# Kernel tuning notes

Measured on AMD Instinct MI355X. Metric: run time of the kernel, lower is better.

Reference implementation:

```python
import jax, jax.numpy as jnp
import numpy as np

H = 1024   # hidden_size
NH = 16    # num heads
DH = H // NH
L = 2      # attention levels
E = 8      # experts
F = 4 * H  # expert FFN hidden
B = 2
S = 1024
EPS = 1e-5
TOPK = 2
STD = 0.02


def setup_inputs() -> dict:
    key = jax.random.key(0)
    ks = jax.random.split(key, 12)
    def n(k, shp):
        return jax.random.normal(k, shp, jnp.float32) * STD
    return {
        "hidden_states": jax.random.normal(ks[0], (B, S, H), jnp.float32),
        "attention_mask": jnp.ones((B, S), jnp.int32),
        "ln1_g": jnp.ones((H,), jnp.float32), "ln1_b": jnp.zeros((H,), jnp.float32),
        "ln2_g": jnp.ones((H,), jnp.float32), "ln2_b": jnp.zeros((H,), jnp.float32),
        "Wq": n(ks[1], (L, H, H)), "Wk": n(ks[2], (L, H, H)),
        "Wv": n(ks[3], (L, H, H)), "Wo": n(ks[4], (L, H, H)),
        "bq": jnp.zeros((L, H), jnp.float32), "bk": jnp.zeros((L, H), jnp.float32),
        "bv": jnp.zeros((L, H), jnp.float32), "bo": jnp.zeros((L, H), jnp.float32),
        "level_logits": n(ks[5], (L,)),
        "Wr": n(ks[6], (H, E)), "br": jnp.zeros((E,), jnp.float32),
        "W1": n(ks[7], (E, H, F)), "b1": jnp.zeros((E, F), jnp.float32),
        "W2": n(ks[8], (E, F, H)), "b2": jnp.zeros((E, H), jnp.float32),
    }


def _ln(x, g, b):
    m = x.mean(-1, keepdims=True)
    v = x.var(-1, keepdims=True)
    return (x - m) * jax.lax.rsqrt(v + EPS) * g + b


def _mla(x, mask_f, Wq, Wk, Wv, Wo, bq, bk, bv, bo, level_logits):
    # Multi-level attention: one MHA per level, softmax-combined over levels.
    b_, s_, _ = x.shape
    def proj(W, bias):
        y = jnp.einsum('bsh,lhd->lbsd', x, W) + bias[:, None, None, :]
        return y.reshape(L, b_, s_, NH, DH)
    q, k, v = proj(Wq, bq), proj(Wk, bk), proj(Wv, bv)
    scores = jnp.einsum('lbqnd,lbknd->lbnqk', q, k) / np.float32(np.sqrt(DH))
    bias = (1.0 - mask_f)[None, :, None, None, :] * jnp.float32(-1e9)  # key-side mask
    attn = jax.nn.softmax(scores + bias, axis=-1)
    ctx = jnp.einsum('lbnqk,lbknd->lbqnd', attn, v).reshape(L, b_, s_, H)
    out = jnp.einsum('lbsh,lhd->lbsd', ctx, Wo) + bo[:, None, None, :]
    w = jax.nn.softmax(level_logits)
    return jnp.einsum('l,lbsd->bsd', w, out)


def _moe(x, Wr, br, W1, b1, W2, b2):
    # Top-2 softmax router with renormalized gates; dense expert compute,
    # sparse combine (math-equivalent to dispatch/combine without dropping).
    logits = x @ Wr + br                                  # [B,S,E]
    probs = jax.nn.softmax(logits, axis=-1)
    topv, topi = jax.lax.top_k(probs, TOPK)               # [B,S,K]
    gates = topv / topv.sum(-1, keepdims=True)
    combine = jnp.sum(jax.nn.one_hot(topi, E, dtype=x.dtype) * gates[..., None], axis=-2)  # [B,S,E]
    h = jax.nn.gelu(jnp.einsum('bsh,ehf->besf', x, W1) + b1[None, :, None, :])
    y = jnp.einsum('besf,efh->besh', h, W2) + b2[None, :, None, :]
    return jnp.einsum('bse,besh->bsh', combine, y), logits


def reference(hidden_states, attention_mask, ln1_g, ln1_b, ln2_g, ln2_b,
              Wq, Wk, Wv, Wo, bq, bk, bv, bo, level_logits,
              Wr, br, W1, b1, W2, b2):
    mask_f = attention_mask.astype(jnp.float32)
    attn = _mla(_ln(hidden_states, ln1_g, ln1_b), mask_f,
                Wq, Wk, Wv, Wo, bq, bk, bv, bo, level_logits)
    x = hidden_states + attn                  # residual 1 (dropout in eval = identity)
    moe_out, _router_logits = _moe(_ln(x, ln2_g, ln2_b), Wr, br, W1, b1, W2, b2)
    return x + moe_out                        # residual 2
```

## Files before the change

kernel.cpp:

```cpp
#include <hip/hip_runtime.h>
#include <hip/hip_bf16.h>
#include <stdint.h>

#define Hn   1024
#define NHn  16
#define DHn  64
#define Ln   2
#define En   8
#define Fn   4096
#define Bn   2
#define Sn   1024
#define Tn   2048
#define An   4096
#define KSPLIT 4

typedef __bf16 bf16_t;
typedef __bf16 bf16x8 __attribute__((ext_vector_type(8)));
typedef float  f32x4  __attribute__((ext_vector_type(4)));

__device__ __forceinline__ f32x4 mfma16(bf16x8 a, bf16x8 b, f32x4 c){
  return __builtin_amdgcn_mfma_f32_16x16x32_bf16(a, b, c, 0, 0, 0);
}
__device__ __forceinline__ void gload16(const void* gsrc, void* ldst){
  __builtin_amdgcn_global_load_lds((const __attribute__((address_space(1))) void*)gsrc,
                                   (__attribute__((address_space(3))) void*)ldst, 16, 0, 0);
}
__device__ __forceinline__ float gelu_f(float x){
  float u = 0.7978845608028654f * (x + 0.044715f * x * x * x);
  return 0.5f * x * (1.0f + tanhf(u));
}

__global__ __launch_bounds__(256)
void tcvt_k(const float* __restrict__ src, bf16_t* __restrict__ dst, int R, int C){
  __shared__ float tile[32][33];
  size_t moff = (size_t)blockIdx.z * R * C;
  src += moff; dst += moff;
  int c0 = blockIdx.x * 32, r0 = blockIdx.y * 32;
  int tx = threadIdx.x & 31, ty = threadIdx.x >> 5;
  #pragma unroll
  for (int i = 0; i < 32; i += 8)
    tile[ty + i][tx] = src[(size_t)(r0 + ty + i) * C + (c0 + tx)];
  __syncthreads();
  #pragma unroll
  for (int i = 0; i < 32; i += 8)
    dst[(size_t)(c0 + ty + i) * R + (r0 + tx)] = (bf16_t)tile[tx][ty + i];
}

__global__ __launch_bounds__(256)
void ln_k(const float* __restrict__ x, const float* __restrict__ gam,
          const float* __restrict__ bet, bf16_t* __restrict__ out){
  int row = blockIdx.x;
  const float4* xr = (const float4*)(x + (size_t)row * Hn);
  int t = threadIdx.x, lane = t & 63, w = t >> 6;
  float4 v = xr[t];
  float s  = v.x + v.y + v.z + v.w;
  float ss = v.x*v.x + v.y*v.y + v.z*v.z + v.w*v.w;
  #pragma unroll
  for (int mk = 1; mk < 64; mk <<= 1){ s += __shfl_xor(s, mk); ss += __shfl_xor(ss, mk); }
  __shared__ float r1[4], r2[4];
  if (lane == 0){ r1[w] = s; r2[w] = ss; }
  __syncthreads();
  float S1 = r1[0]+r1[1]+r1[2]+r1[3];
  float S2 = r2[0]+r2[1]+r2[2]+r2[3];
  float mean = S1 * (1.0f/Hn);
  float var  = S2 * (1.0f/Hn) - mean*mean;
  float rstd = rsqrtf(var + 1e-5f);
  int c = t * 4;
  bf16_t* o = out + (size_t)row * Hn + c;
  o[0] = (bf16_t)((v.x-mean)*rstd*gam[c+0] + bet[c+0]);
  o[1] = (bf16_t)((v.y-mean)*rstd*gam[c+1] + bet[c+1]);
  o[2] = (bf16_t)((v.z-mean)*rstd*gam[c+2] + bet[c+2]);
  o[3] = (bf16_t)((v.w-mean)*rstd*gam[c+3] + bet[c+3]);
}

__global__ __launch_bounds__(256)
void res_ln2_k(const float* __restrict__ x, const float* __restrict__ o0,
               const float* __restrict__ o1, const float* __restrict__ lvl,
               const float* __restrict__ gam, const float* __restrict__ bet,
               float* __restrict__ x2, bf16_t* __restrict__ xn2){
  int row = blockIdx.x, t = threadIdx.x, lane = t & 63, w = t >> 6;
  float l0 = lvl[0], l1 = lvl[1];
  float mx = fmaxf(l0, l1);
  float e0 = __expf(l0 - mx), e1 = __expf(l1 - mx);
  float inv = 1.f / (e0 + e1);
  float w0 = e0 * inv, w1 = e1 * inv;
  size_t base = (size_t)row * Hn;
  float4 xv = ((const float4*)(x  + base))[t];
  float4 a0 = ((const float4*)(o0 + base))[t];
  float4 a1 = ((const float4*)(o1 + base))[t];
  float4 v;
  v.x = xv.x + w0*a0.x + w1*a1.x;
  v.y = xv.y + w0*a0.y + w1*a1.y;
  v.z = xv.z + w0*a0.z + w1*a1.z;
  v.w = xv.w + w0*a0.w + w1*a1.w;
  ((float4*)(x2 + base))[t] = v;
  float s  = v.x + v.y + v.z + v.w;
  float ss = v.x*v.x + v.y*v.y + v.z*v.z + v.w*v.w;
  #pragma unroll
  for (int mk = 1; mk < 64; mk <<= 1){ s += __shfl_xor(s, mk); ss += __shfl_xor(ss, mk); }
  __shared__ float r1[4], r2[4];
  if (lane == 0){ r1[w] = s; r2[w] = ss; }
  __syncthreads();
  float S1 = r1[0]+r1[1]+r1[2]+r1[3];
  float S2 = r2[0]+r2[1]+r2[2]+r2[3];
  float mean = S1 * (1.0f/Hn);
  float var  = S2 * (1.0f/Hn) - mean*mean;
  float rstd = rsqrtf(var + 1e-5f);
  int c = t * 4;
  bf16_t* o = xn2 + base + c;
  o[0] = (bf16_t)((v.x-mean)*rstd*gam[c+0] + bet[c+0]);
  o[1] = (bf16_t)((v.y-mean)*rstd*gam[c+1] + bet[c+1]);
  o[2] = (bf16_t)((v.z-mean)*rstd*gam[c+2] + bet[c+2]);
  o[3] = (bf16_t)((v.w-mean)*rstd*gam[c+3] + bet[c+3]);
}

struct GP {
  const bf16_t* A;
  const bf16_t* Bt;
  const float*  bias;
  float*        fout;
  bf16_t*       bfout;
  const int*    list;
  const int*    counts;
  int Kstride;
  int Kloc;
};

template<int MODE>
__global__ __launch_bounds__(256)
void gemm_k(GP p){
  const int nt = blockIdx.x, mt = blockIdx.y, z = blockIdx.z;
  const bf16_t* A = p.A;
  const bf16_t* Bt = p.Bt;
  const float* bias = p.bias;
  const int* list = nullptr;
  int cnt = 0x7fffffff;
  int kbase = 0;
  if constexpr (MODE == 0){
    Bt += (size_t)z*Hn*Hn; bias += z*Hn;
  } else if constexpr (MODE == 1){
    Bt += (size_t)z*Hn*Hn; bias += z*Hn; A += (size_t)z*Bn*Sn*Hn;
  } else if constexpr (MODE == 3){
    cnt = p.counts[z];
    if (mt * 128 >= cnt) return;
    list = p.list + z * Tn;
    Bt += (size_t)z*Fn*Hn; bias += z*Fn;
  } else {
    int e = z >> 2;
    cnt = p.counts[e];
    if (mt * 128 >= cnt) return;
    list = p.list + e * Tn;
    Bt += (size_t)e*Hn*Fn; bias += e*Hn;
    kbase = (z & 3) * (Fn / KSPLIT);
  }
  const int Ks = p.Kstride;
  const int NT = p.Kloc >> 5;

  __shared__ bf16_t As[2][128*32];
  __shared__ bf16_t Bs[2][128*32];
  const int tid = threadIdx.x, lane = tid & 63, w = tid >> 6;
  const int wr = (w >> 1) * 64, wc = (w & 1) * 64;
  const int lane15 = lane & 15, kg = lane >> 4;

  const bf16_t* aptr[2];
  const bf16_t* bptr[2];
  int chunks[2];
  #pragma unroll
  for (int i = 0; i < 2; ++i){
    int ch = w*64 + lane + i*256;
    chunks[i] = ch;
    int row = ch >> 2, kc = (ch & 3) * 8;
    int ar;
    if constexpr (MODE == 3){ int g = mt*128 + row; if (g >= cnt) g = cnt - 1; ar = list[g] >> 1; }
    else if constexpr (MODE == 4){ int g = mt*128 + row; if (g >= cnt) g = cnt - 1; ar = list[g]; }
    else ar = mt*128 + row;
    aptr[i] = A  + (size_t)ar * Ks + kbase + kc;
    bptr[i] = Bt + (size_t)(nt*128 + row) * Ks + kbase + kc;
  }

  const f32x4 fz = {0.f,0.f,0.f,0.f};
  f32x4 acc[4][4];
  #pragma unroll
  for (int m = 0; m < 4; ++m)
    #pragma unroll
    for (int n = 0; n < 4; ++n) acc[m][n] = fz;

  #pragma unroll
  for (int i = 0; i < 2; ++i){
    gload16(aptr[i], &As[0][chunks[i]*8]);
    gload16(bptr[i], &Bs[0][chunks[i]*8]);
  }
  __syncthreads();

  int cur = 0;
  for (int t = 0; t < NT; ++t){
    if (t + 1 < NT){
      int k1 = (t+1) * 32;
      #pragma unroll
      for (int i = 0; i < 2; ++i){
        gload16(aptr[i] + k1, &As[cur^1][chunks[i]*8]);
        gload16(bptr[i] + k1, &Bs[cur^1][chunks[i]*8]);
      }
    }
    bf16x8 af[4], bfr[4];
    #pragma unroll
    for (int m = 0; m < 4; ++m) af[m]  = *(const bf16x8*)(&As[cur][(wr + m*16 + lane15)*32 + kg*8]);
    #pragma unroll
    for (int n = 0; n < 4; ++n) bfr[n] = *(const bf16x8*)(&Bs[cur][(wc + n*16 + lane15)*32 + kg*8]);
    #pragma unroll
    for (int m = 0; m < 4; ++m)
      #pragma unroll
      for (int n = 0; n < 4; ++n)
        acc[m][n] = mfma16(af[m], bfr[n], acc[m][n]);
    __syncthreads();
    cur ^= 1;
  }

  if constexpr (MODE == 0){
    bf16_t* outp = p.bfout + (size_t)z * (Bn*NHn*Sn*DHn);
    #pragma unroll
    for (int m = 0; m < 4; ++m){
      int row0 = mt*128 + wr + m*16 + kg*4;
      #pragma unroll
      for (int n = 0; n < 4; ++n){
        int col = nt*128 + wc + n*16 + lane15;
        int nh = col >> 6, dh = col & 63;
        float bv = bias[col];
        f32x4 v = acc[m][n];
        #pragma unroll
        for (int r = 0; r < 4; ++r){
          int tk = row0 + r;
          int bb = tk >> 10, s = tk & 1023;
          outp[((size_t)(bb*NHn + nh)*Sn + s)*DHn + dh] = (bf16_t)(v[r] + bv);
        }
      }
    }
  } else if constexpr (MODE == 1){
    float* outp = p.fout + (size_t)z * Tn * Hn;
    #pragma unroll
    for (int m = 0; m < 4; ++m){
      int row0 = mt*128 + wr + m*16 + kg*4;
      #pragma unroll
      for (int n = 0; n < 4; ++n){
        int col = nt*128 + wc + n*16 + lane15;
        float bv = bias[col];
        f32x4 v = acc[m][n];
        #pragma unroll
        for (int r = 0; r < 4; ++r)
          outp[(size_t)(row0 + r)*Hn + col] = v[r] + bv;
      }
    }
  } else if constexpr (MODE == 3){
    #pragma unroll
    for (int m = 0; m < 4; ++m){
      int row0 = mt*128 + wr + m*16 + kg*4;
      #pragma unroll
      for (int n = 0; n < 4; ++n){
        int col = nt*128 + wc + n*16 + lane15;
        float bv = bias[col];
        f32x4 v = acc[m][n];
        #pragma unroll
        for (int r = 0; r < 4; ++r){
          int g = row0 + r;
          if (g < cnt){
            int aid = list[g];
            p.bfout[(size_t)aid*Fn + col] = (bf16_t)gelu_f(v[r] + bv);
          }
        }
      }
    }
  } else {
    float* outp = p.fout + (size_t)(z & 3) * An * Hn;
    bool addb = (z & 3) == 0;
    #pragma unroll
    for (int m = 0; m < 4; ++m){
      int row0 = mt*128 + wr + m*16 + kg*4;
      #pragma unroll
      for (int n = 0; n < 4; ++n){
        int col = nt*128 + wc + n*16 + lane15;
        float bv = addb ? bias[col] : 0.f;
        f32x4 v = acc[m][n];
        #pragma unroll
        for (int r = 0; r < 4; ++r){
          int g = row0 + r;
          if (g < cnt){
            int aid = list[g];
            outp[(size_t)aid*Hn + col] = v[r] + bv;
          }
        }
      }
    }
  }
}

__global__ __launch_bounds__(64)
void attn_k(const bf16_t* __restrict__ qh, const bf16_t* __restrict__ kh,
            const bf16_t* __restrict__ vh, const int* __restrict__ amask,
            bf16_t* __restrict__ ctxb){
  int qt = blockIdx.x;
  int z  = blockIdx.y;
  int lvl = z >> 5, bb = (z >> 4) & 1, nh = z & 15;
  int lane = threadIdx.x;
  int lane15 = lane & 15, kg = lane >> 4;
  const bf16_t* Q  = qh + (size_t)z * Sn * DHn;
  const bf16_t* Kp = kh + (size_t)z * Sn * DHn;
  const bf16_t* Vp = vh + (size_t)z * Sn * DHn;
  const int* mrow = amask + bb * Sn;
  __shared__ bf16_t p_lds[16*32];
  __shared__ bf16_t vt[64*32];
  const f32x4 fz = {0.f,0.f,0.f,0.f};
  int qr = qt*16 + lane15;
  bf16x8 qa0 = *(const bf16x8*)(Q + (size_t)qr*DHn + kg*8);
  bf16x8 qa1 = *(const bf16x8*)(Q + (size_t)qr*DHn + 32 + kg*8);
  f32x4 ctxa[4] = {fz, fz, fz, fz};
  float m_r[4] = {-1e30f,-1e30f,-1e30f,-1e30f};
  float s_r[4] = {0.f,0.f,0.f,0.f};
  int vr = lane >> 1, c0 = (lane & 1) * 32;
  for (int kc = 0; kc < 32; ++kc){
    int k0 = kc * 32;
    bf16x8 ka0 = *(const bf16x8*)(Kp + (size_t)(k0+lane15)*DHn + kg*8);
    bf16x8 ka1 = *(const bf16x8*)(Kp + (size_t)(k0+lane15)*DHn + 32 + kg*8);
    bf16x8 kb0 = *(const bf16x8*)(Kp + (size_t)(k0+16+lane15)*DHn + kg*8);
    bf16x8 kb1 = *(const bf16x8*)(Kp + (size_t)(k0+16+lane15)*DHn + 32 + kg*8);
    f32x4 sA = mfma16(qa1, ka1, mfma16(qa0, ka0, fz));
    f32x4 sB = mfma16(qa1, kb1, mfma16(qa0, kb0, fz));
    float bias0 = mrow[k0 + lane15]      ? 0.f : -1e9f;
    float bias1 = mrow[k0 + 16 + lane15] ? 0.f : -1e9f;
    const bf16x8* vsrc = (const bf16x8*)(Vp + (size_t)(k0+vr)*DHn + c0);
    bf16x8 vv0 = vsrc[0], vv1 = vsrc[1], vv2 = vsrc[2], vv3 = vsrc[3];
    #pragma unroll
    for (int r = 0; r < 4; ++r){
      float sa = sA[r]*0.125f + bias0;
      float sb = sB[r]*0.125f + bias1;
      float mx = fmaxf(sa, sb);
      #pragma unroll
      for (int mk = 1; mk < 16; mk <<= 1) mx = fmaxf(mx, __shfl_xor(mx, mk));
      float mnew = fmaxf(m_r[r], mx);
      float corr = __expf(m_r[r] - mnew);
      float pa = __expf(sa - mnew);
      float pb = __expf(sb - mnew);
      float rs = pa + pb;
      #pragma unroll
      for (int mk = 1; mk < 16; mk <<= 1) rs += __shfl_xor(rs, mk);
      s_r[r] = s_r[r]*corr + rs;
      m_r[r] = mnew;
      ctxa[0][r] *= corr; ctxa[1][r] *= corr; ctxa[2][r] *= corr; ctxa[3][r] *= corr;
      p_lds[(kg*4 + r)*32 + lane15]      = (bf16_t)pa;
      p_lds[(kg*4 + r)*32 + 16 + lane15] = (bf16_t)pb;
    }
    #pragma unroll
    for (int j = 0; j < 8; ++j){
      vt[(c0 + j     )*32 + vr] = vv0[j];
      vt[(c0 + 8  + j)*32 + vr] = vv1[j];
      vt[(c0 + 16 + j)*32 + vr] = vv2[j];
      vt[(c0 + 24 + j)*32 + vr] = vv3[j];
    }
    __syncthreads();
    bf16x8 paf = *(const bf16x8*)(p_lds + lane15*32 + kg*8);
    #pragma unroll
    for (int df = 0; df < 4; ++df){
      bf16x8 vbf = *(const bf16x8*)(vt + (size_t)(df*16 + lane15)*32 + kg*8);
      ctxa[df] = mfma16(paf, vbf, ctxa[df]);
    }
    __syncthreads();
  }
  #pragma unroll
  for (int df = 0; df < 4; ++df){
    #pragma unroll
    for (int r = 0; r < 4; ++r){
      int srow = qt*16 + kg*4 + r;
      int d = df*16 + lane15;
      ctxb[((size_t)(lvl*2 + bb)*Sn + srow)*Hn + nh*DHn + d] = (bf16_t)(ctxa[df][r] / s_r[r]);
    }
  }
}

__global__ __launch_bounds__(64)
void router_k(const float* __restrict__ x2, const float* __restrict__ gam,
              const float* __restrict__ bet, const float* __restrict__ Wr,
              const float* __restrict__ br, float* __restrict__ gates,
              int* __restrict__ lists, int* __restrict__ counts){
  int t = blockIdx.x, lane = threadIdx.x;
  const float4* xr = (const float4*)(x2 + (size_t)t * Hn);
  float4 vbuf[4];
  float s = 0.f, ss = 0.f;
  #pragma unroll
  for (int i = 0; i < 4; ++i){
    float4 v = xr[lane + i*64];
    vbuf[i] = v;
    s  += v.x + v.y + v.z + v.w;
    ss += v.x*v.x + v.y*v.y + v.z*v.z + v.w*v.w;
  }
  #pragma unroll
  for (int mk = 1; mk < 64; mk <<= 1){ s += __shfl_xor(s, mk); ss += __shfl_xor(ss, mk); }
  float mean = s * (1.0f/Hn);
  float var  = ss * (1.0f/Hn) - mean*mean;
  float rstd = rsqrtf(var + 1e-5f);
  float a[8] = {0,0,0,0,0,0,0,0};
  #pragma unroll
  for (int i = 0; i < 4; ++i){
    int c = (lane + i*64) * 4;
    float4 v = vbuf[i];
    float xn[4] = {
      (v.x-mean)*rstd*gam[c+0] + bet[c+0],
      (v.y-mean)*rstd*gam[c+1] + bet[c+1],
      (v.z-mean)*rstd*gam[c+2] + bet[c+2],
      (v.w-mean)*rstd*gam[c+3] + bet[c+3]};
    #pragma unroll
    for (int j = 0; j < 4; ++j){
      const float* w = Wr + (size_t)(c + j) * En;
      #pragma unroll
      for (int e8 = 0; e8 < 8; ++e8) a[e8] += xn[j] * w[e8];
    }
  }
  #pragma unroll
  for (int e8 = 0; e8 < 8; ++e8)
    #pragma unroll
    for (int mk = 1; mk < 64; mk <<= 1) a[e8] += __shfl_xor(a[e8], mk);
  if (lane == 0){
    float lg[8]; float mx = -1e30f;
    #pragma unroll
    for (int e8 = 0; e8 < 8; ++e8){ lg[e8] = a[e8] + br[e8]; mx = fmaxf(mx, lg[e8]); }
    float p[8];
    #pragma unroll
    for (int e8 = 0; e8 < 8; ++e8) p[e8] = __expf(lg[e8] - mx);
    int i0 = 0; float v0 = p[0];
    #pragma unroll
    for (int e8 = 1; e8 < 8; ++e8) if (p[e8] > v0){ v0 = p[e8]; i0 = e8; }
    int i1 = -1; float v1 = -1.f;
    #pragma unroll
    for (int e8 = 0; e8 < 8; ++e8) if (e8 != i0 && p[e8] > v1){ v1 = p[e8]; i1 = e8; }
    float g0 = v0 / (v0 + v1), g1 = v1 / (v0 + v1);
    gates[2*t] = g0; gates[2*t+1] = g1;
    int s0 = atomicAdd(&counts[i0], 1); lists[i0*Tn + s0] = 2*t;
    int s1 = atomicAdd(&counts[i1], 1); lists[i1*Tn + s1] = 2*t + 1;
  }
}

__global__ __launch_bounds__(256)
void comb_k(const float* __restrict__ x2, const float* __restrict__ P,
            const float* __restrict__ gates, float* __restrict__ out){
  int t = blockIdx.x, i = threadIdx.x;
  float g0 = gates[2*t], g1 = gates[2*t+1];
  const size_t PS = (size_t)An * Hn;
  f32x4 s0 = {0,0,0,0}, s1 = {0,0,0,0};
  #pragma unroll
  for (int ks = 0; ks < KSPLIT; ++ks){
    f32x4 u0 = ((const f32x4*)(P + ks*PS + (size_t)(2*t)*Hn))[i];
    f32x4 u1 = ((const f32x4*)(P + ks*PS + (size_t)(2*t+1)*Hn))[i];
    s0 += u0; s1 += u1;
  }
  f32x4 va = ((const f32x4*)(x2 + (size_t)t*Hn))[i];
  f32x4 o = va + g0*s0 + g1*s1;
  ((f32x4*)(out + (size_t)t*Hn))[i] = o;
}

extern "C" void kernel_launch(void* const* d_in, const int* in_sizes, int n_in,
                              void* d_out, int out_size, void* d_ws, size_t ws_size,
                              hipStream_t stream)
{
  const float* x    = (const float*)d_in[0];
  const int* amask  = (const int*)d_in[1];
  const float* ln1g = (const float*)d_in[2];
  const float* ln1b = (const float*)d_in[3];
  const float* ln2g = (const float*)d_in[4];
  const float* ln2b = (const float*)d_in[5];
  const float* Wq   = (const float*)d_in[6];
  const float* Wk   = (const float*)d_in[7];
  const float* Wv   = (const float*)d_in[8];
  const float* Wo   = (const float*)d_in[9];
  const float* bq   = (const float*)d_in[10];
  const float* bk   = (const float*)d_in[11];
  const float* bv   = (const float*)d_in[12];
  const float* bo   = (const float*)d_in[13];
  const float* lvl  = (const float*)d_in[14];
  const float* Wr   = (const float*)d_in[15];
  const float* br   = (const float*)d_in[16];
  const float* W1   = (const float*)d_in[17];
  const float* b1   = (const float*)d_in[18];
  const float* W2   = (const float*)d_in[19];
  const float* b2   = (const float*)d_in[20];
  float* out = (float*)d_out;
  (void)in_sizes; (void)n_in; (void)out_size; (void)ws_size;

  char* wsp = (char*)d_ws;
  auto nxt = [&](size_t bytes) -> char* {
    char* r = wsp; wsp += (bytes + 255) & ~(size_t)255; return r;
  };
  bf16_t* wqkvT = (bf16_t*)nxt((size_t)6*Hn*Hn*2);
  bf16_t* woT   = (bf16_t*)nxt((size_t)Ln*Hn*Hn*2);
  bf16_t* w1t   = (bf16_t*)nxt((size_t)En*Fn*Hn*2);
  bf16_t* w2t   = (bf16_t*)nxt((size_t)En*Hn*Fn*2);
  float*  bqkv  = (float*)nxt((size_t)6*Hn*4);
  bf16_t* xn1   = (bf16_t*)nxt((size_t)Tn*Hn*2);
  bf16_t* qkvh  = (bf16_t*)nxt((size_t)6*Bn*NHn*Sn*DHn*2);
  bf16_t* ctxb  = (bf16_t*)nxt((size_t)Ln*Bn*Sn*Hn*2);
  float*  otmp  = (float*)nxt((size_t)Ln*Tn*Hn*4);
  float*  x2    = (float*)nxt((size_t)Tn*Hn*4);
  bf16_t* xn2   = (bf16_t*)nxt((size_t)Tn*Hn*2);
  float*  gates = (float*)nxt((size_t)Tn*2*4);
  int*    lists = (int*)nxt((size_t)En*Tn*4);
  int*    counts= (int*)nxt(256);
  bf16_t* hbuf  = (bf16_t*)nxt((size_t)An*Fn*2);
  float*  ybuf  = (float*)nxt((size_t)KSPLIT*An*Hn*4);

  hipMemsetAsync(counts, 0, En*sizeof(int), stream);
  hipMemcpyAsync(bqkv,          bq, (size_t)Ln*Hn*4, hipMemcpyDeviceToDevice, stream);
  hipMemcpyAsync(bqkv + 2*Hn,   bk, (size_t)Ln*Hn*4, hipMemcpyDeviceToDevice, stream);
  hipMemcpyAsync(bqkv + 4*Hn,   bv, (size_t)Ln*Hn*4, hipMemcpyDeviceToDevice, stream);

  tcvt_k<<<dim3(32,32,Ln), 256, 0, stream>>>(Wq, wqkvT,            Hn, Hn);
  tcvt_k<<<dim3(32,32,Ln), 256, 0, stream>>>(Wk, wqkvT + 2*Hn*Hn,  Hn, Hn);
  tcvt_k<<<dim3(32,32,Ln), 256, 0, stream>>>(Wv, wqkvT + 4*Hn*Hn,  Hn, Hn);
  tcvt_k<<<dim3(32,32,Ln), 256, 0, stream>>>(Wo, woT,              Hn, Hn);
  tcvt_k<<<dim3(Fn/32, Hn/32, En), 256, 0, stream>>>(W1, w1t, Hn, Fn);
  tcvt_k<<<dim3(Hn/32, Fn/32, En), 256, 0, stream>>>(W2, w2t, Fn, Hn);

  ln_k<<<Tn, 256, 0, stream>>>(x, ln1g, ln1b, xn1);

  { GP g{};
    g.A = xn1; g.Bt = wqkvT; g.bias = bqkv; g.bfout = qkvh;
    g.Kstride = Hn; g.Kloc = Hn;
    gemm_k<0><<<dim3(8,16,6), 256, 0, stream>>>(g); }

  {
    const bf16_t* qh = qkvh;
    const bf16_t* kh = qkvh + (size_t)2*Bn*NHn*Sn*DHn;
    const bf16_t* vh = qkvh + (size_t)4*Bn*NHn*Sn*DHn;
    attn_k<<<dim3(Sn/16, Ln*Bn*NHn), 64, 0, stream>>>(qh, kh, vh, amask, ctxb);
  }

  { GP g{};
    g.A = ctxb; g.Bt = woT; g.bias = bo; g.fout = otmp;
    g.Kstride = Hn; g.Kloc = Hn;
    gemm_k<1><<<dim3(8,16,2), 256, 0, stream>>>(g); }

  res_ln2_k<<<Tn, 256, 0, stream>>>(x, otmp, otmp + (size_t)Tn*Hn, lvl,
                                    ln2g, ln2b, x2, xn2);
  router_k<<<Tn, 64, 0, stream>>>(x2, ln2g, ln2b, Wr, br, gates, lists, counts);

  { GP g{};
    g.A = xn2; g.Bt = w1t; g.bias = b1; g.bfout = hbuf;
    g.list = lists; g.counts = counts;
    g.Kstride = Hn; g.Kloc = Hn;
    gemm_k<3><<<dim3(Fn/128, 16, En), 256, 0, stream>>>(g); }
  { GP g{};
    g.A = hbuf; g.Bt = w2t; g.bias = b2; g.fout = ybuf;
    g.list = lists; g.counts = counts;
    g.Kstride = Fn; g.Kloc = Fn / KSPLIT;
    gemm_k<4><<<dim3(Hn/128, 16, En*KSPLIT), 256, 0, stream>>>(g); }

  comb_k<<<Tn, 256, 0, stream>>>(x2, ybuf, gates, out);
}
```

Before: 539.0 us.

## Write V transposed from QKV GEMM and restructure attention softmax per lane

The QKV projection epilogue now writes V in a [head, dim, seq] transposed layout with packed 4-wide bf16 stores. The attention kernel then reads V fragments straight from global memory, dropping the per-chunk LDS transpose and both barriers. Scores are computed transposed so each lane owns one query row, which removes most cross-lane shuffle reductions. The max rescale is skipped when no row's max grows, and the mask bias is precomputed into LDS. The grid is also swapped so consecutive blocks share the same head's K/V in cache. The trade is more uncoalesced global reads for V fragments and more complex bookkeeping for the running max and sum.

```diff
diff --git a/kernel.cpp b/kernel.cpp
--- a/kernel.cpp
+++ b/kernel.cpp
@@ -15,6 +15,8 @@
 #define KSPLIT 4
 
 typedef __bf16 bf16_t;
+typedef __bf16 bf16x2 __attribute__((ext_vector_type(2)));
+typedef __bf16 bf16x4 __attribute__((ext_vector_type(4)));
 typedef __bf16 bf16x8 __attribute__((ext_vector_type(8)));
 typedef float  f32x4  __attribute__((ext_vector_type(4)));
 
@@ -218,20 +220,41 @@
 
   if constexpr (MODE == 0){
     bf16_t* outp = p.bfout + (size_t)z * (Bn*NHn*Sn*DHn);
-    #pragma unroll
-    for (int m = 0; m < 4; ++m){
-      int row0 = mt*128 + wr + m*16 + kg*4;
-      #pragma unroll
-      for (int n = 0; n < 4; ++n){
-        int col = nt*128 + wc + n*16 + lane15;
-        int nh = col >> 6, dh = col & 63;
-        float bv = bias[col];
-        f32x4 v = acc[m][n];
+    if (z < 4){
+      #pragma unroll
+      for (int m = 0; m < 4; ++m){
+        int row0 = mt*128 + wr + m*16 + kg*4;
         #pragma unroll
-        for (int r = 0; r < 4; ++r){
-          int tk = row0 + r;
-          int bb = tk >> 10, s = tk & 1023;
-          outp[((size_t)(bb*NHn + nh)*Sn + s)*DHn + dh] = (bf16_t)(v[r] + bv);
+        for (int n = 0; n < 4; ++n){
+          int col = nt*128 + wc + n*16 + lane15;
+          int nh = col >> 6, dh = col & 63;
+          float bv = bias[col];
+          f32x4 v = acc[m][n];
+          #pragma unroll
+          for (int r = 0; r < 4; ++r){
+            int tk = row0 + r;
+            int bb = tk >> 10, s = tk & 1023;
+            outp[((size_t)(bb*NHn + nh)*Sn + s)*DHn + dh] = (bf16_t)(v[r] + bv);
+          }
+        }
+      }
+    } else {
+      #pragma unroll
+      for (int m = 0; m < 4; ++m){
+        int row0 = mt*128 + wr + m*16 + kg*4;
+        int bb = row0 >> 10, s = row0 & 1023;
+        #pragma unroll
+        for (int n = 0; n < 4; ++n){
+          int col = nt*128 + wc + n*16 + lane15;
+          int nh = col >> 6, dh = col & 63;
+          float bv = bias[col];
+          f32x4 v = acc[m][n];
+          bf16x4 pk;
+          pk[0] = (bf16_t)(v[0] + bv);
+          pk[1] = (bf16_t)(v[1] + bv);
+          pk[2] = (bf16_t)(v[2] + bv);
+          pk[3] = (bf16_t)(v[3] + bv);
+          *(bf16x4*)(outp + ((size_t)(bb*NHn + nh)*DHn + dh)*Sn + s) = pk;
         }
       }
     }
@@ -295,82 +318,96 @@
 
 __global__ __launch_bounds__(64)
 void attn_k(const bf16_t* __restrict__ qh, const bf16_t* __restrict__ kh,
-            const bf16_t* __restrict__ vh, const int* __restrict__ amask,
+            const bf16_t* __restrict__ vtb, const int* __restrict__ amask,
             bf16_t* __restrict__ ctxb){
-  int qt = blockIdx.x;
-  int z  = blockIdx.y;
+  int z  = blockIdx.x;
+  int qt = blockIdx.y;
   int lvl = z >> 5, bb = (z >> 4) & 1, nh = z & 15;
   int lane = threadIdx.x;
   int lane15 = lane & 15, kg = lane >> 4;
-  const bf16_t* Q  = qh + (size_t)z * Sn * DHn;
-  const bf16_t* Kp = kh + (size_t)z * Sn * DHn;
-  const bf16_t* Vp = vh + (size_t)z * Sn * DHn;
+  const bf16_t* Q  = qh  + (size_t)z * Sn * DHn;
+  const bf16_t* Kp = kh  + (size_t)z * Sn * DHn;
+  const bf16_t* Vt = vtb + (size_t)z * DHn * Sn;
   const int* mrow = amask + bb * Sn;
-  __shared__ bf16_t p_lds[16*32];
-  __shared__ bf16_t vt[64*32];
+  __shared__ float bias_lds[Sn];
+  __shared__ bf16_t p_lds[16*40];
+  for (int i = lane; i < Sn/4; i += 64){
+    int4 mv = ((const int4*)mrow)[i];
+    float4 bv;
+    bv.x = mv.x ? 0.f : -1e9f;
+    bv.y = mv.y ? 0.f : -1e9f;
+    bv.z = mv.z ? 0.f : -1e9f;
+    bv.w = mv.w ? 0.f : -1e9f;
+    ((float4*)bias_lds)[i] = bv;
+  }
   const f32x4 fz = {0.f,0.f,0.f,0.f};
   int qr = qt*16 + lane15;
   bf16x8 qa0 = *(const bf16x8*)(Q + (size_t)qr*DHn + kg*8);
   bf16x8 qa1 = *(const bf16x8*)(Q + (size_t)qr*DHn + 32 + kg*8);
   f32x4 ctxa[4] = {fz, fz, fz, fz};
-  float m_r[4] = {-1e30f,-1e30f,-1e30f,-1e30f};
-  float s_r[4] = {0.f,0.f,0.f,0.f};
-  int vr = lane >> 1, c0 = (lane & 1) * 32;
+  float m_ln = -1e30f;
+  float s_ln = 0.f;
+  float m_out[4] = {-1e30f,-1e30f,-1e30f,-1e30f};
   for (int kc = 0; kc < 32; ++kc){
     int k0 = kc * 32;
     bf16x8 ka0 = *(const bf16x8*)(Kp + (size_t)(k0+lane15)*DHn + kg*8);
     bf16x8 ka1 = *(const bf16x8*)(Kp + (size_t)(k0+lane15)*DHn + 32 + kg*8);
     bf16x8 kb0 = *(const bf16x8*)(Kp + (size_t)(k0+16+lane15)*DHn + kg*8);
     bf16x8 kb1 = *(const bf16x8*)(Kp + (size_t)(k0+16+lane15)*DHn + 32 + kg*8);
-    f32x4 sA = mfma16(qa1, ka1, mfma16(qa0, ka0, fz));
-    f32x4 sB = mfma16(qa1, kb1, mfma16(qa0, kb0, fz));
-    float bias0 = mrow[k0 + lane15]      ? 0.f : -1e9f;
-    float bias1 = mrow[k0 + 16 + lane15] ? 0.f : -1e9f;
-    const bf16x8* vsrc = (const bf16x8*)(Vp + (size_t)(k0+vr)*DHn + c0);
-    bf16x8 vv0 = vsrc[0], vv1 = vsrc[1], vv2 = vsrc[2], vv3 = vsrc[3];
-    #pragma unroll
-    for (int r = 0; r < 4; ++r){
-      float sa = sA[r]*0.125f + bias0;
-      float sb = sB[r]*0.125f + bias1;
-      float mx = fmaxf(sa, sb);
-      #pragma unroll
-      for (int mk = 1; mk < 16; mk <<= 1) mx = fmaxf(mx, __shfl_xor(mx, mk));
-      float mnew = fmaxf(m_r[r], mx);
-      float corr = __expf(m_r[r] - mnew);
-      float pa = __expf(sa - mnew);
-      float pb = __expf(sb - mnew);
-      float rs = pa + pb;
-      #pragma unroll
-      for (int mk = 1; mk < 16; mk <<= 1) rs += __shfl_xor(rs, mk);
-      s_r[r] = s_r[r]*corr + rs;
-      m_r[r] = mnew;
-      ctxa[0][r] *= corr; ctxa[1][r] *= corr; ctxa[2][r] *= corr; ctxa[3][r] *= corr;
-      p_lds[(kg*4 + r)*32 + lane15]      = (bf16_t)pa;
-      p_lds[(kg*4 + r)*32 + 16 + lane15] = (bf16_t)pb;
-    }
-    #pragma unroll
-    for (int j = 0; j < 8; ++j){
-      vt[(c0 + j     )*32 + vr] = vv0[j];
-      vt[(c0 + 8  + j)*32 + vr] = vv1[j];
-      vt[(c0 + 16 + j)*32 + vr] = vv2[j];
-      vt[(c0 + 24 + j)*32 + vr] = vv3[j];
-    }
-    __syncthreads();
-    bf16x8 paf = *(const bf16x8*)(p_lds + lane15*32 + kg*8);
+    f32x4 sA = mfma16(ka1, qa1, mfma16(ka0, qa0, fz));
+    f32x4 sB = mfma16(kb1, qa1, mfma16(kb0, qa0, fz));
+    float4 biasA = *(const float4*)(bias_lds + k0 + kg*4);
+    float4 biasB = *(const float4*)(bias_lds + k0 + 16 + kg*4);
+    float sv[8];
+    sv[0] = sA[0]*0.125f + biasA.x;
+    sv[1] = sA[1]*0.125f + biasA.y;
+    sv[2] = sA[2]*0.125f + biasA.z;
+    sv[3] = sA[3]*0.125f + biasA.w;
+    sv[4] = sB[0]*0.125f + biasB.x;
+    sv[5] = sB[1]*0.125f + biasB.y;
+    sv[6] = sB[2]*0.125f + biasB.z;
+    sv[7] = sB[3]*0.125f + biasB.w;
+    float mx = fmaxf(fmaxf(fmaxf(sv[0],sv[1]),fmaxf(sv[2],sv[3])),
+                     fmaxf(fmaxf(sv[4],sv[5]),fmaxf(sv[6],sv[7])));
+    mx = fmaxf(mx, __shfl_xor(mx, 16));
+    mx = fmaxf(mx, __shfl_xor(mx, 32));
+    if (!__all(mx <= m_ln)){
+      float mnew = fmaxf(m_ln, mx);
+      s_ln *= __expf(m_ln - mnew);
+      #pragma unroll
+      for (int r = 0; r < 4; ++r){
+        float mo = __shfl(mnew, kg*4 + r);
+        float corr = __expf(m_out[r] - mo);
+        ctxa[0][r] *= corr; ctxa[1][r] *= corr; ctxa[2][r] *= corr; ctxa[3][r] *= corr;
+        m_out[r] = mo;
+      }
+      m_ln = mnew;
+    }
+    float pv[8];
+    #pragma unroll
+    for (int j = 0; j < 8; ++j){ pv[j] = __expf(sv[j] - m_ln); s_ln += pv[j]; }
+    bf16_t* pr = p_lds + lane15*40;
+    *(bf16x2*)(pr + kg*4)          = (bf16x2){(bf16_t)pv[0], (bf16_t)pv[1]};
+    *(bf16x2*)(pr + kg*4 + 2)      = (bf16x2){(bf16_t)pv[2], (bf16_t)pv[3]};
+    *(bf16x2*)(pr + 16 + kg*4)     = (bf16x2){(bf16_t)pv[4], (bf16_t)pv[5]};
+    *(bf16x2*)(pr + 16 + kg*4 + 2) = (bf16x2){(bf16_t)pv[6], (bf16_t)pv[7]};
+    bf16x8 paf = *(const bf16x8*)(p_lds + lane15*40 + kg*8);
     #pragma unroll
     for (int df = 0; df < 4; ++df){
-      bf16x8 vbf = *(const bf16x8*)(vt + (size_t)(df*16 + lane15)*32 + kg*8);
+      bf16x8 vbf = *(const bf16x8*)(Vt + (size_t)(df*16 + lane15)*Sn + k0 + kg*8);
       ctxa[df] = mfma16(paf, vbf, ctxa[df]);
     }
-    __syncthreads();
-  }
-  #pragma unroll
-  for (int df = 0; df < 4; ++df){
-    #pragma unroll
-    for (int r = 0; r < 4; ++r){
-      int srow = qt*16 + kg*4 + r;
+  }
+  s_ln += __shfl_xor(s_ln, 16);
+  s_ln += __shfl_xor(s_ln, 32);
+  #pragma unroll
+  for (int r = 0; r < 4; ++r){
+    float inv = 1.f / __shfl(s_ln, kg*4 + r);
+    int srow = qt*16 + kg*4 + r;
+    #pragma unroll
+    for (int df = 0; df < 4; ++df){
       int d = df*16 + lane15;
-      ctxb[((size_t)(lvl*2 + bb)*Sn + srow)*Hn + nh*DHn + d] = (bf16_t)(ctxa[df][r] / s_r[r]);
+      ctxb[((size_t)(lvl*2 + bb)*Sn + srow)*Hn + nh*DHn + d] = (bf16_t)(ctxa[df][r] * inv);
     }
   }
 }
@@ -526,8 +563,8 @@
   {
     const bf16_t* qh = qkvh;
     const bf16_t* kh = qkvh + (size_t)2*Bn*NHn*Sn*DHn;
-    const bf16_t* vh = qkvh + (size_t)4*Bn*NHn*Sn*DHn;
-    attn_k<<<dim3(Sn/16, Ln*Bn*NHn), 64, 0, stream>>>(qh, kh, vh, amask, ctxb);
+    const bf16_t* vt = qkvh + (size_t)4*Bn*NHn*Sn*DHn;
+    attn_k<<<dim3(Ln*Bn*NHn, Sn/16), 64, 0, stream>>>(qh, kh, vt, amask, ctxb);
   }
 
   { GP g{};
```

After: 560.1 us. 1.04x slower.
